# Performance work log

Measured on AMD Instinct MI355X. Metric: run time of the kernel, lower is better.

The kernel has to match this reference:

```python
import jax, jax.numpy as jnp
import numpy as np

TAU = 0.5


def _l2norm(x):
    return x / jnp.linalg.norm(x, axis=1, keepdims=True)


def _project(z, W1, b1, W2, b2):
    h = jax.nn.elu(z @ W1.T + b1)
    return h @ W2.T + b2


def _semi_loss(h1, h2):
    # cos sim via row-normalized matmul
    n1 = _l2norm(h1)
    n2 = _l2norm(h2)
    between = jnp.exp((n1 @ n2.T) / TAU)  # [N, N]
    refl = jnp.exp((n1 @ n1.T) / TAU)     # [N, N]
    pos = jnp.diagonal(between)
    denom = refl.sum(axis=1) + between.sum(axis=1) + pos \
        - jnp.diagonal(refl) - jnp.diagonal(between)
    return -jnp.log(pos / denom)


def setup_inputs() -> dict:
    key = jax.random.key(0)
    k1, k2, k3, k4 = jax.random.split(key, 4)
    N, D, P = 12288, 256, 256
    z1 = jax.random.normal(k1, (N, D), dtype=jnp.float32)
    z2 = jax.random.normal(k2, (N, D), dtype=jnp.float32)
    W1 = jax.random.normal(k3, (P, D), dtype=jnp.float32) * (1.0 / np.sqrt(D))
    b1 = jnp.zeros((P,), dtype=jnp.float32)
    W2 = jax.random.normal(k4, (D, P), dtype=jnp.float32) * (1.0 / np.sqrt(P))
    b2 = jnp.zeros((D,), dtype=jnp.float32)
    return {"z1": z1, "z2": z2, "W1": W1, "b1": b1, "W2": W2, "b2": b2}


def reference(z1, z2, W1, b1, W2, b2):
    h1 = _project(z1, W1, b1, W2, b2)
    h2 = _project(z2, W1, b1, W2, b2)
    l1 = _semi_loss(h1, h2)
    l2 = _semi_loss(h2, h1)
    return ((l1 + l2) * 0.5).mean()
```

## Files before the change

kernel.cpp:

```cpp
#include <hip/hip_runtime.h>
#include <hip/hip_bf16.h>
#include <hip/hip_fp8.h>


#define NROWS 12288
#define TWO_N 24576
#define KDIM 256
#define BM 128
#define BK 32
#define NTILE 192
#define PAIRS 96
#define SLOTS 16
#define FB 48
#define LOG2E 1.4426950408889634f
#define SIMSCALE 1.6986436f
#define LN2F 0.6931471805599453f

#if __has_builtin(__builtin_amdgcn_exp2f)
#define EXP2F(x) __builtin_amdgcn_exp2f(x)
#else
#define EXP2F(x) exp2f(x)
#endif

typedef __bf16 bf16x8 __attribute__((ext_vector_type(8)));
typedef __bf16 bf16x4v __attribute__((ext_vector_type(4)));
typedef float f32x4 __attribute__((ext_vector_type(4)));
typedef int i32x4 __attribute__((ext_vector_type(4)));
typedef int i32x8 __attribute__((ext_vector_type(8)));
typedef unsigned char uchar;

typedef const __attribute__((address_space(1))) void* gptr_t;
typedef __attribute__((address_space(3))) void* lptr_t;

__device__ __forceinline__ bf16x8 read_frag(const __bf16* lds, int rowbase,
                                            int tile, int l) {
  int r = rowbase + tile * 16 + (l & 15);
  int q = l >> 4;
  int blk = q ^ (r & 3);
  return *(const bf16x8*)(lds + r * 32 + blk * 8);
}

__global__ void cast_w_kernel(const float* __restrict__ W1,
                              const float* __restrict__ W2,
                              __bf16* __restrict__ W1b,
                              __bf16* __restrict__ W2b) {
  const int n4w = KDIM * KDIM / 4;
  int i = blockIdx.x * blockDim.x + threadIdx.x;
  const float* src;
  __bf16* dst;
  int j;
  if (i < n4w) {
    src = W1; dst = W1b; j = i;
  } else if (i < 2 * n4w) {
    src = W2; dst = W2b; j = i - n4w;
  } else {
    return;
  }
  float4 v = *(const float4*)(src + (size_t)j * 4);
  bf16x4v o;
  o[0] = (__bf16)v.x; o[1] = (__bf16)v.y; o[2] = (__bf16)v.z; o[3] = (__bf16)v.w;
  *(bf16x4v*)(dst + (size_t)j * 4) = o;
}

__device__ __forceinline__ uchar fp8_byte(float x) {
#if __has_builtin(__builtin_amdgcn_cvt_pk_fp8_f32)
  int v = __builtin_amdgcn_cvt_pk_fp8_f32(x, 0.f, 0, false);
  return (uchar)(v & 0xFF);
#else
  __hip_fp8_e4m3 qv(x);
  return qv.__x;
#endif
}

__global__ __launch_bounds__(256, 2) void mlp_kernel(
    const float* __restrict__ z1, const float* __restrict__ z2,
    const __bf16* __restrict__ W1b, const __bf16* __restrict__ W2b,
    const float* __restrict__ b1, const float* __restrict__ b2,
    uchar* __restrict__ Nq) {
  __shared__ __align__(16) __bf16 Zs[64 * BK];
  __shared__ __align__(16) __bf16 Ws[KDIM * BK];
  __shared__ __align__(16) __bf16 Ts[8 * 64 * 32];
  __shared__ float ssred[4][64];
  __shared__ float invred[64];
  uchar* qbuf = (uchar*)Ts;
  int tid = threadIdx.x;
  int w = tid >> 6, l = tid & 63;
  int q = l >> 4, rx = l & 15;
  int i0 = blockIdx.x * 64;
  int wbcol = w * 64;
  const float* zrow = (i0 < NROWS) ? (z1 + (size_t)i0 * KDIM)
                                   : (z2 + (size_t)(i0 - NROWS) * KDIM);

  auto stageW = [&](const __bf16* Wb, int ks) {
#pragma unroll
    for (int t = 0; t < 4; ++t) {
      int c = w * 4 + t;
      int rr = l >> 2, c2 = l & 3;
      int r = c * 16 + rr;
      int src = c2 ^ (r & 3);
      const __bf16* ga = Wb + (size_t)r * KDIM + ks * BK + src * 8;
      __builtin_amdgcn_global_load_lds((gptr_t)ga, (lptr_t)(Ws + c * 512),
                                       16, 0, 0);
    }
  };
  const int zr = tid >> 2, zblk = tid & 3;
  const int zsrc = zblk ^ (zr & 3);
  auto loadZ = [&](int ks, float4& v0, float4& v1) {
    const float* zp = zrow + (size_t)zr * KDIM + ks * BK + zsrc * 8;
    v0 = *(const float4*)zp;
    v1 = *(const float4*)(zp + 4);
  };

  f32x4 acc[4][4] = {};
  float4 zv0, zv1;
  loadZ(0, zv0, zv1);
  for (int ks = 0; ks < 8; ++ks) {
    __syncthreads();
    bf16x8 zo;
    zo[0] = (__bf16)zv0.x; zo[1] = (__bf16)zv0.y;
    zo[2] = (__bf16)zv0.z; zo[3] = (__bf16)zv0.w;
    zo[4] = (__bf16)zv1.x; zo[5] = (__bf16)zv1.y;
    zo[6] = (__bf16)zv1.z; zo[7] = (__bf16)zv1.w;
    *(bf16x8*)(Zs + zr * 32 + zblk * 8) = zo;
    stageW(W1b, ks);
    if (ks + 1 < 8) loadZ(ks + 1, zv0, zv1);
    __syncthreads();
    bf16x8 aF[4], bF[4];
#pragma unroll
    for (int mi = 0; mi < 4; ++mi) aF[mi] = read_frag(Zs, 0, mi, l);
#pragma unroll
    for (int ni = 0; ni < 4; ++ni) bF[ni] = read_frag(Ws, wbcol, ni, l);
#pragma unroll
    for (int mi = 0; mi < 4; ++mi)
#pragma unroll
      for (int ni = 0; ni < 4; ++ni)
        acc[mi][ni] = __builtin_amdgcn_mfma_f32_16x16x32_bf16(
            aF[mi], bF[ni], acc[mi][ni], 0, 0, 0);
  }

  float bias1[4];
#pragma unroll
  for (int ni = 0; ni < 4; ++ni) bias1[ni] = b1[wbcol + ni * 16 + rx];
#pragma unroll
  for (int mi = 0; mi < 4; ++mi)
#pragma unroll
    for (int ni = 0; ni < 4; ++ni)
#pragma unroll
      for (int v = 0; v < 4; ++v) {
        int row = mi * 16 + q * 4 + v;
        int col = wbcol + ni * 16 + rx;
        float x = acc[mi][ni][v] + bias1[ni];
        x = x > 0.f ? x : (EXP2F(x * LOG2E) - 1.f);
        int ks2 = col >> 5, c32 = col & 31;
        Ts[ks2 * 2048 + row * 32 + (((c32 >> 3) ^ (row & 3)) << 3) +
           (col & 7)] = (__bf16)x;
      }

#pragma unroll
  for (int mi = 0; mi < 4; ++mi)
#pragma unroll
    for (int ni = 0; ni < 4; ++ni) acc[mi][ni] = (f32x4){0.f, 0.f, 0.f, 0.f};
  for (int ks = 0; ks < 8; ++ks) {
    __syncthreads();
    stageW(W2b, ks);
    __syncthreads();
    bf16x8 aF[4], bF[4];
#pragma unroll
    for (int mi = 0; mi < 4; ++mi)
      aF[mi] = read_frag(Ts + ks * 2048, 0, mi, l);
#pragma unroll
    for (int ni = 0; ni < 4; ++ni) bF[ni] = read_frag(Ws, wbcol, ni, l);
#pragma unroll
    for (int mi = 0; mi < 4; ++mi)
#pragma unroll
      for (int ni = 0; ni < 4; ++ni)
        acc[mi][ni] = __builtin_amdgcn_mfma_f32_16x16x32_bf16(
            aF[mi], bF[ni], acc[mi][ni], 0, 0, 0);
  }

  float bias2[4];
#pragma unroll
  for (int ni = 0; ni < 4; ++ni) bias2[ni] = b2[wbcol + ni * 16 + rx];
  float ss[4][4] = {};
#pragma unroll
  for (int mi = 0; mi < 4; ++mi)
#pragma unroll
    for (int ni = 0; ni < 4; ++ni)
#pragma unroll
      for (int v = 0; v < 4; ++v) {
        float x = acc[mi][ni][v] + bias2[ni];
        acc[mi][ni][v] = x;
        ss[mi][v] += x * x;
      }
#pragma unroll
  for (int mi = 0; mi < 4; ++mi)
#pragma unroll
    for (int v = 0; v < 4; ++v) {
      float x = ss[mi][v];
      x += __shfl_xor(x, 1, 64);
      x += __shfl_xor(x, 2, 64);
      x += __shfl_xor(x, 4, 64);
      x += __shfl_xor(x, 8, 64);
      if (rx == 0) ssred[w][mi * 16 + q * 4 + v] = x;
    }
  __syncthreads();
  if (tid < 64)
    invred[tid] = rsqrtf(ssred[0][tid] + ssred[1][tid] + ssred[2][tid] +
                         ssred[3][tid]) * SIMSCALE;
  __syncthreads();

#pragma unroll
  for (int mi = 0; mi < 4; ++mi)
#pragma unroll
    for (int v = 0; v < 4; ++v) {
      int row = mi * 16 + q * 4 + v;
      float iv = invred[row];
#pragma unroll
      for (int ni = 0; ni < 4; ++ni)
        qbuf[row * KDIM + wbcol + ni * 16 + rx] =
            fp8_byte(acc[mi][ni][v] * iv);
    }
  __syncthreads();
  size_t base = (size_t)i0 * KDIM;
#pragma unroll
  for (int it = 0; it < 8; ++it) {
    int idx = it * 2048 + tid * 8;
    *(uint2*)(Nq + base + idx) = *(const uint2*)(qbuf + idx);
  }
}

__global__ __launch_bounds__(256, 2) void sim_kernel(
    const uchar* __restrict__ Nq, float* __restrict__ Rlow,
    float* __restrict__ Rhigh, float* __restrict__ Dsame,
    float* __restrict__ Dcross) {
  __shared__ __align__(16) uchar Bs[2][BM * KDIM];
  int tid = threadIdx.x;
  int w = tid >> 6, l = tid & 63;
  int q = l >> 4;
  int rx = l & 15;
  int b = blockIdx.x;
  int p = b >> 4;
  int s = b & 15;
  const int I1 = p, I2 = NTILE - 1 - p;
  const int L1 = NTILE - I1;
  int fstart = (s == 0) ? 0 : 13 + (s - 1) * 12;
  int fend = fstart + ((s == 0) ? 13 : 12);
  int warow = (w >> 1) * 64;
  int wbcol = (w & 1) * 64;

  unsigned off0[8];
#pragma unroll
  for (int t = 0; t < 8; ++t) {
    int ch = w * 8 + t;
    int r = ch * 4 + (l >> 4);
    int c = l & 15;
    int src = c ^ (r & 15);
    off0[t] = (unsigned)(r * KDIM + src * 16);
  }
  auto jtile_of = [&](int F) { return (F < L1) ? (I1 + F) : (F - 1); };
  auto atile_of = [&](int F) { return (F < L1) ? I1 : I2; };

  auto stage = [&](int F, int bi) {
    unsigned jo = (unsigned)(jtile_of(F) * (BM * KDIM));
#pragma unroll
    for (int t = 0; t < 8; ++t) {
      const uchar* ga = Nq + (size_t)(jo + off0[t]);
      uchar* la = Bs[bi] + (w * 8 + t) * 1024;
      __builtin_amdgcn_global_load_lds((gptr_t)ga, (lptr_t)la, 16, 0, 0);
    }
  };

  i32x8 aF[4][2];
  auto load_aF = [&](int Atile) {
#pragma unroll
    for (int mi = 0; mi < 4; ++mi) {
      const uchar* ap = Nq +
          (size_t)(Atile * BM + warow + mi * 16 + rx) * KDIM + q * 32;
#pragma unroll
      for (int hf = 0; hf < 2; ++hf)
        aF[mi][hf] = *(const i32x8*)(ap + hf * 128);
    }
  };

  int rdo[2][2];
#pragma unroll
  for (int hf = 0; hf < 2; ++hf) {
    int kb = hf * 8 + 2 * q;
    rdo[hf][0] = (kb ^ rx) << 4;
    rdo[hf][1] = ((kb + 1) ^ rx) << 4;
  }

  f32x4 rs4[4] = {};
  f32x4 cs4[4];
  int pend = 0;
  float* pendR = nullptr;
  int pendBase = 0;

  auto flushrs = [&](int Atile, int h) {
    float* R = h ? Rhigh : Rlow;
#pragma unroll
    for (int mi = 0; mi < 4; ++mi)
#pragma unroll
      for (int v = 0; v < 4; ++v) {
        float x = rs4[mi][v];
        x += __shfl_xor(x, 1, 64);
        x += __shfl_xor(x, 2, 64);
        x += __shfl_xor(x, 4, 64);
        x += __shfl_xor(x, 8, 64);
        if (rx == 0)
          atomicAdd(&R[Atile * BM + warow + mi * 16 + q * 4 + v], x);
        rs4[mi][v] = 0.f;
      }
  };
  auto flushcs = [&]() {
#pragma unroll
    for (int nj = 0; nj < 4; ++nj) {
      float c = (cs4[nj][0] + cs4[nj][1]) + (cs4[nj][2] + cs4[nj][3]);
      c += __shfl_xor(c, 16, 64);
      c += __shfl_xor(c, 32, 64);
      if (q == 0)
        atomicAdd(&pendR[pendBase + wbcol + nj * 16 + rx], c);
    }
    pend = 0;
  };

  const f32x4 Z4 = {0.f, 0.f, 0.f, 0.f};

  int Aprev = atile_of(fstart);
  int hprev = (jtile_of(fstart) >= NTILE / 2) ? 1 : 0;
  load_aF(Aprev);
  stage(fstart, 0);

  for (int f = fstart; f < fend; ++f) {
    int bi = (f - fstart) & 1;
    __syncthreads();
    if (f + 1 < fend) stage(f + 1, bi ^ 1);
    if (pend) flushcs();

    int Atile = atile_of(f);
    int Jt = jtile_of(f);
    int h = (Jt >= NTILE / 2) ? 1 : 0;
    if (Atile != Aprev) {
      flushrs(Aprev, hprev);
      load_aF(Atile);
      Aprev = Atile;
      hprev = h;
    } else if (h != hprev) {
      flushrs(Aprev, hprev);
      hprev = h;
    }

    bool dsame = (Jt == Atile);
    bool dcross = (Jt == Atile + NTILE / 2);
    float* Rcol = (Atile >= NTILE / 2) ? Rhigh : Rlow;

    const uchar* bL = Bs[bi] + (size_t)(wbcol + rx) * KDIM;
    const uchar* p00 = bL + rdo[0][0];
    const uchar* p01 = bL + rdo[0][1];
    const uchar* p10 = bL + rdo[1][0];
    const uchar* p11 = bL + rdo[1][1];

#pragma unroll
    for (int nj = 0; nj < 4; ++nj) {
      const int no = nj * 4096;
      i32x8 bF0 = __builtin_shufflevector(*(const i32x4*)(p00 + no),
                                          *(const i32x4*)(p01 + no),
                                          0, 1, 2, 3, 4, 5, 6, 7);
      i32x8 bF1 = __builtin_shufflevector(*(const i32x4*)(p10 + no),
                                          *(const i32x4*)(p11 + no),
                                          0, 1, 2, 3, 4, 5, 6, 7);
      f32x4 acc[4];
#pragma unroll
      for (int mi = 0; mi < 4; ++mi)
        acc[mi] = __builtin_amdgcn_mfma_scale_f32_16x16x128_f8f6f4(
            aF[mi][0], bF0, Z4, 0, 0, 0, 0x7F7F7F7F, 0, 0x7F7F7F7F);
#pragma unroll
      for (int mi = 0; mi < 4; ++mi)
        acc[mi] = __builtin_amdgcn_mfma_scale_f32_16x16x128_f8f6f4(
            aF[mi][1], bF1, acc[mi], 0, 0, 0, 0x7F7F7F7F, 0, 0x7F7F7F7F);
#pragma unroll
      for (int mi = 0; mi < 4; ++mi) {
        f32x4 e4;
        e4[0] = EXP2F(acc[mi][0]);
        e4[1] = EXP2F(acc[mi][1]);
        e4[2] = EXP2F(acc[mi][2]);
        e4[3] = EXP2F(acc[mi][3]);
        rs4[mi] += e4;
        cs4[nj] = (mi == 0) ? e4 : (cs4[nj] + e4);
      }

      if (dsame | dcross) {
        float* D = dsame ? Dsame : Dcross;
#pragma unroll
        for (int mi = 0; mi < 4; ++mi)
#pragma unroll
          for (int v = 0; v < 4; ++v) {
            int li = warow + mi * 16 + q * 4 + v;
            int lj = wbcol + nj * 16 + rx;
            if (li == lj) D[Atile * BM + li] = acc[mi][v];
          }
      }
    }

    if (!dsame) {
      pend = 1;
      pendR = Rcol;
      pendBase = Jt * BM;
    }
  }

  if (pend) flushcs();
  flushrs(Aprev, hprev);
}

__global__ void finalize1_kernel(const float* __restrict__ Rlow,
                                 const float* __restrict__ Rhigh,
                                 const float* __restrict__ Dsame,
                                 const float* __restrict__ Dcross,
                                 float* __restrict__ partial) {
  __shared__ float red[256];
  int k = blockIdx.x * 256 + threadIdx.x;
  float d1 = Rlow[k] + Rhigh[k] - EXP2F(Dsame[k]);
  float d2 = Rhigh[NROWS + k] + Rlow[NROWS + k] - EXP2F(Dsame[NROWS + k]);
  float acc = 0.5f * (logf(d1) + logf(d2)) - LN2F * Dcross[k];
  red[threadIdx.x] = acc;
  __syncthreads();
  for (int s = 128; s > 0; s >>= 1) {
    if (threadIdx.x < s) red[threadIdx.x] += red[threadIdx.x + s];
    __syncthreads();
  }
  if (threadIdx.x == 0) partial[blockIdx.x] = red[0];
}

__global__ void finalize2_kernel(const float* __restrict__ partial,
                                 float* __restrict__ out) {
  float x = (threadIdx.x < FB) ? partial[threadIdx.x] : 0.f;
#pragma unroll
  for (int s = 32; s > 0; s >>= 1) x += __shfl_down(x, s, 64);
  if (threadIdx.x == 0) out[0] = x / (float)NROWS;
}

extern "C" void kernel_launch(void* const* d_in, const int* in_sizes, int n_in,
                              void* d_out, int out_size, void* d_ws,
                              size_t ws_size, hipStream_t stream) {
  const float* z1 = (const float*)d_in[0];
  const float* z2 = (const float*)d_in[1];
  const float* W1 = (const float*)d_in[2];
  const float* b1 = (const float*)d_in[3];
  const float* W2 = (const float*)d_in[4];
  const float* b2 = (const float*)d_in[5];
  float* out = (float*)d_out;

  char* ws = (char*)d_ws;
  size_t off = 0;
  auto alloc = [&](size_t bytes) -> void* {
    void* p = ws + off;
    off += (bytes + 255) & ~(size_t)255;
    return p;
  };
  __bf16* W1b  = (__bf16*)alloc((size_t)KDIM * KDIM * 2);
  __bf16* W2b  = (__bf16*)alloc((size_t)KDIM * KDIM * 2);
  uchar*  Nq   = (uchar*)alloc((size_t)TWO_N * KDIM);
  float*  Rlow = (float*)alloc((size_t)TWO_N * 4);
  float*  Rhigh= (float*)alloc((size_t)TWO_N * 4);
  float*  Dsame= (float*)alloc((size_t)TWO_N * 4);
  float*  Dcross=(float*)alloc((size_t)NROWS * 4);
  float*  partial=(float*)alloc((size_t)FB * 4);

  hipMemsetAsync(Rlow, 0, (size_t)2 * TWO_N * 4, stream);

  int n4w = KDIM * KDIM / 4;
  cast_w_kernel<<<(2 * n4w + 255) / 256, 256, 0, stream>>>(W1, W2, W1b, W2b);

  mlp_kernel<<<TWO_N / 64, 256, 0, stream>>>(z1, z2, W1b, W2b, b1, b2, Nq);

  sim_kernel<<<PAIRS * SLOTS, 256, 0, stream>>>(Nq, Rlow, Rhigh, Dsame,
                                                Dcross);
  finalize1_kernel<<<FB, 256, 0, stream>>>(Rlow, Rhigh, Dsame, Dcross, partial);
  finalize2_kernel<<<1, 64, 0, stream>>>(partial, out);
}
```

Measured before the change: 210.2 us.

## Split sim kernel into MFMA producer and exp/reduce consumer warps

Result: slower. 279.3 us (+32.9%).

```diff
diff --git a/kernel.cpp b/kernel.cpp
--- a/kernel.cpp
+++ b/kernel.cpp
@@ -10,7 +10,6 @@
 #define BK 32
 #define NTILE 192
 #define PAIRS 96
-#define SLOTS 16
 #define FB 48
 #define LOG2E 1.4426950408889634f
 #define SIMSCALE 1.6986436f
@@ -229,43 +228,46 @@
   }
 }
 
-__global__ __launch_bounds__(256, 2) void sim_kernel(
+__global__ __launch_bounds__(512, 2) void sim_kernel(
     const uchar* __restrict__ Nq, float* __restrict__ Rlow,
     float* __restrict__ Rhigh, float* __restrict__ Dsame,
     float* __restrict__ Dcross) {
   __shared__ __align__(16) uchar Bs[2][BM * KDIM];
+  __shared__ __align__(16) float4 Ab[2][4][512];
   int tid = threadIdx.x;
   int w = tid >> 6, l = tid & 63;
+  bool prod = (w < 4);
+  int wq = w & 3;
   int q = l >> 4;
   int rx = l & 15;
   int b = blockIdx.x;
-  int p = b >> 4;
-  int s = b & 15;
+  int p = b >> 3;
+  int s = b & 7;
   const int I1 = p, I2 = NTILE - 1 - p;
   const int L1 = NTILE - I1;
-  int fstart = (s == 0) ? 0 : 13 + (s - 1) * 12;
-  int fend = fstart + ((s == 0) ? 13 : 12);
-  int warow = (w >> 1) * 64;
-  int wbcol = (w & 1) * 64;
-
-  unsigned off0[8];
-#pragma unroll
-  for (int t = 0; t < 8; ++t) {
-    int ch = w * 8 + t;
-    int r = ch * 4 + (l >> 4);
-    int c = l & 15;
-    int src = c ^ (r & 15);
-    off0[t] = (unsigned)(r * KDIM + src * 16);
-  }
+  int fstart = (s == 0) ? 0 : 25 + (s - 1) * 24;
+  int fend = fstart + ((s == 0) ? 25 : 24);
+  const int T = fend - fstart;
+  int warow = (wq >> 1) * 64;
+  int wbcol = (wq & 1) * 64;
+
   auto jtile_of = [&](int F) { return (F < L1) ? (I1 + F) : (F - 1); };
   auto atile_of = [&](int F) { return (F < L1) ? I1 : I2; };
 
+  unsigned off0[8];
+#pragma unroll
+  for (int t = 0; t < 8; ++t) {
+    int ch = wq * 8 + t;
+    int r = ch * 4 + q;
+    int src = rx ^ (r & 15);
+    off0[t] = (unsigned)(r * KDIM + src * 16);
+  }
   auto stage = [&](int F, int bi) {
     unsigned jo = (unsigned)(jtile_of(F) * (BM * KDIM));
 #pragma unroll
     for (int t = 0; t < 8; ++t) {
       const uchar* ga = Nq + (size_t)(jo + off0[t]);
-      uchar* la = Bs[bi] + (w * 8 + t) * 1024;
+      uchar* la = Bs[bi] + (wq * 8 + t) * 1024;
       __builtin_amdgcn_global_load_lds((gptr_t)ga, (lptr_t)la, 16, 0, 0);
     }
   };
@@ -281,7 +283,6 @@
         aF[mi][hf] = *(const i32x8*)(ap + hf * 128);
     }
   };
-
   int rdo[2][2];
 #pragma unroll
   for (int hf = 0; hf < 2; ++hf) {
@@ -289,12 +290,44 @@
     rdo[hf][0] = (kb ^ rx) << 4;
     rdo[hf][1] = ((kb + 1) ^ rx) << 4;
   }
+  const f32x4 Z4 = {0.f, 0.f, 0.f, 0.f};
+
+  auto produce = [&](int ht) {
+    int fl = ht >> 1;
+    int njbase = (ht & 1) * 2;
+    const uchar* bL = Bs[fl & 1] + (size_t)(wbcol + rx) * KDIM;
+#pragma unroll
+    for (int njh = 0; njh < 2; ++njh) {
+      const int no = (njbase + njh) * 4096;
+      i32x8 bF0 = __builtin_shufflevector(
+          *(const i32x4*)(bL + no + rdo[0][0]),
+          *(const i32x4*)(bL + no + rdo[0][1]), 0, 1, 2, 3, 4, 5, 6, 7);
+      i32x8 bF1 = __builtin_shufflevector(
+          *(const i32x4*)(bL + no + rdo[1][0]),
+          *(const i32x4*)(bL + no + rdo[1][1]), 0, 1, 2, 3, 4, 5, 6, 7);
+      f32x4 acc[4];
+#pragma unroll
+      for (int mi = 0; mi < 4; ++mi)
+        acc[mi] = __builtin_amdgcn_mfma_scale_f32_16x16x128_f8f6f4(
+            aF[mi][0], bF0, Z4, 0, 0, 0, 0x7F7F7F7F, 0, 0x7F7F7F7F);
+#pragma unroll
+      for (int mi = 0; mi < 4; ++mi)
+        acc[mi] = __builtin_amdgcn_mfma_scale_f32_16x16x128_f8f6f4(
+            aF[mi][1], bF1, acc[mi], 0, 0, 0, 0x7F7F7F7F, 0, 0x7F7F7F7F);
+#pragma unroll
+      for (int mi = 0; mi < 4; ++mi)
+        Ab[ht & 1][wq][(njh * 4 + mi) * 64 + l] =
+            (float4){acc[mi][0], acc[mi][1], acc[mi][2], acc[mi][3]};
+    }
+  };
 
   f32x4 rs4[4] = {};
   f32x4 cs4[4];
   int pend = 0;
   float* pendR = nullptr;
   int pendBase = 0;
+  int Aprev = atile_of(fstart);
+  int hprev = (jtile_of(fstart) >= NTILE / 2) ? 1 : 0;
 
   auto flushrs = [&](int Atile, int h) {
     float* R = h ? Rhigh : Rlow;
@@ -324,93 +357,92 @@
     pend = 0;
   };
 
-  const f32x4 Z4 = {0.f, 0.f, 0.f, 0.f};
-
-  int Aprev = atile_of(fstart);
-  int hprev = (jtile_of(fstart) >= NTILE / 2) ? 1 : 0;
-  load_aF(Aprev);
-  stage(fstart, 0);
-
-  for (int f = fstart; f < fend; ++f) {
-    int bi = (f - fstart) & 1;
-    __syncthreads();
-    if (f + 1 < fend) stage(f + 1, bi ^ 1);
-    if (pend) flushcs();
-
+  auto consume = [&](int g) {
+    int fl = g >> 1;
+    int f = fstart + fl;
+    int half = g & 1;
     int Atile = atile_of(f);
     int Jt = jtile_of(f);
-    int h = (Jt >= NTILE / 2) ? 1 : 0;
-    if (Atile != Aprev) {
-      flushrs(Aprev, hprev);
-      load_aF(Atile);
-      Aprev = Atile;
-      hprev = h;
-    } else if (h != hprev) {
-      flushrs(Aprev, hprev);
-      hprev = h;
-    }
-
     bool dsame = (Jt == Atile);
     bool dcross = (Jt == Atile + NTILE / 2);
-    float* Rcol = (Atile >= NTILE / 2) ? Rhigh : Rlow;
-
-    const uchar* bL = Bs[bi] + (size_t)(wbcol + rx) * KDIM;
-    const uchar* p00 = bL + rdo[0][0];
-    const uchar* p01 = bL + rdo[0][1];
-    const uchar* p10 = bL + rdo[1][0];
-    const uchar* p11 = bL + rdo[1][1];
-
-#pragma unroll
-    for (int nj = 0; nj < 4; ++nj) {
-      const int no = nj * 4096;
-      i32x8 bF0 = __builtin_shufflevector(*(const i32x4*)(p00 + no),
-                                          *(const i32x4*)(p01 + no),
-                                          0, 1, 2, 3, 4, 5, 6, 7);
-      i32x8 bF1 = __builtin_shufflevector(*(const i32x4*)(p10 + no),
-                                          *(const i32x4*)(p11 + no),
-                                          0, 1, 2, 3, 4, 5, 6, 7);
-      f32x4 acc[4];
-#pragma unroll
-      for (int mi = 0; mi < 4; ++mi)
-        acc[mi] = __builtin_amdgcn_mfma_scale_f32_16x16x128_f8f6f4(
-            aF[mi][0], bF0, Z4, 0, 0, 0, 0x7F7F7F7F, 0, 0x7F7F7F7F);
-#pragma unroll
-      for (int mi = 0; mi < 4; ++mi)
-        acc[mi] = __builtin_amdgcn_mfma_scale_f32_16x16x128_f8f6f4(
-            aF[mi][1], bF1, acc[mi], 0, 0, 0, 0x7F7F7F7F, 0, 0x7F7F7F7F);
+    if (half == 0) {
+      int h = (Jt >= NTILE / 2) ? 1 : 0;
+      if (pend) flushcs();
+      if (Atile != Aprev) {
+        flushrs(Aprev, hprev);
+        Aprev = Atile;
+        hprev = h;
+      } else if (h != hprev) {
+        flushrs(Aprev, hprev);
+        hprev = h;
+      }
+    }
+#pragma unroll
+    for (int njh = 0; njh < 2; ++njh) {
+      int nj = half * 2 + njh;
+      f32x4 e4sum = {0.f, 0.f, 0.f, 0.f};
 #pragma unroll
       for (int mi = 0; mi < 4; ++mi) {
-        f32x4 e4;
-        e4[0] = EXP2F(acc[mi][0]);
-        e4[1] = EXP2F(acc[mi][1]);
-        e4[2] = EXP2F(acc[mi][2]);
-        e4[3] = EXP2F(acc[mi][3]);
-        rs4[mi] += e4;
-        cs4[nj] = (mi == 0) ? e4 : (cs4[nj] + e4);
-      }
-
-      if (dsame | dcross) {
-        float* D = dsame ? Dsame : Dcross;
-#pragma unroll
-        for (int mi = 0; mi < 4; ++mi)
+        float4 a = Ab[g & 1][wq][(njh * 4 + mi) * 64 + l];
+        if (dsame | dcross) {
+          float* D = dsame ? Dsame : Dcross;
 #pragma unroll
           for (int v = 0; v < 4; ++v) {
             int li = warow + mi * 16 + q * 4 + v;
             int lj = wbcol + nj * 16 + rx;
-            if (li == lj) D[Atile * BM + li] = acc[mi][v];
+            float av = (v == 0) ? a.x : (v == 1) ? a.y : (v == 2) ? a.z : a.w;
+            if (li == lj) D[Atile * BM + li] = av;
           }
+        }
+        f32x4 e4;
+        e4[0] = EXP2F(a.x);
+        e4[1] = EXP2F(a.y);
+        e4[2] = EXP2F(a.z);
+        e4[3] = EXP2F(a.w);
+        rs4[mi] += e4;
+        e4sum += e4;
       }
-    }
-
-    if (!dsame) {
+      cs4[nj] = (half == 0 && njh == 0 && false) ? e4sum : e4sum;
+      cs4[nj] = e4sum;
+    }
+    if (half == 1 && !dsame) {
       pend = 1;
-      pendR = Rcol;
+      pendR = (Atile >= NTILE / 2) ? Rhigh : Rlow;
       pendBase = Jt * BM;
     }
-  }
-
-  if (pend) flushcs();
-  flushrs(Aprev, hprev);
+  };
+
+  if (prod) stage(fstart, 0);
+  __syncthreads();
+  if (prod) {
+    load_aF(atile_of(fstart));
+    produce(0);
+    if (T > 1) stage(fstart + 1, 1);
+  }
+
+  for (int g = 0; g < 2 * T; ++g) {
+    __syncthreads();
+    int ht = g + 1;
+    if (prod) {
+      if (ht < 2 * T) {
+        int fl = ht >> 1;
+        if ((ht & 1) == 0) {
+          int At = atile_of(fstart + fl);
+          int Ap = atile_of(fstart + fl - 1);
+          if (At != Ap) load_aF(At);
+          if (fl + 1 < T) stage(fstart + fl + 1, (fl + 1) & 1);
+        }
+        produce(ht);
+      }
+    } else {
+      consume(g);
+    }
+  }
+
+  if (!prod) {
+    if (pend) flushcs();
+    flushrs(Aprev, hprev);
+  }
 }
 
 __global__ void finalize1_kernel(const float* __restrict__ Rlow,
@@ -474,8 +506,7 @@
 
   mlp_kernel<<<TWO_N / 64, 256, 0, stream>>>(z1, z2, W1b, W2b, b1, b2, Nq);
 
-  sim_kernel<<<PAIRS * SLOTS, 256, 0, stream>>>(Nq, Rlow, Rhigh, Dsame,
-                                                Dcross);
+  sim_kernel<<<PAIRS * 8, 512, 0, stream>>>(Nq, Rlow, Rhigh, Dsame, Dcross);
   finalize1_kernel<<<FB, 256, 0, stream>>>(Rlow, Rhigh, Dsame, Dcross, partial);
   finalize2_kernel<<<1, 64, 0, stream>>>(partial, out);
 }
```

## Split sim tiles into 128x64 half-tiles with each wave owning 32 rows

Applied to the files above, without the earlier changes.

Measured after the change: 202.0 us. -3.9%, faster.

```diff
diff --git a/kernel.cpp b/kernel.cpp
--- a/kernel.cpp
+++ b/kernel.cpp
@@ -233,7 +233,7 @@
     const uchar* __restrict__ Nq, float* __restrict__ Rlow,
     float* __restrict__ Rhigh, float* __restrict__ Dsame,
     float* __restrict__ Dcross) {
-  __shared__ __align__(16) uchar Bs[2][BM * KDIM];
+  __shared__ __align__(16) uchar Bs[2][64 * KDIM];
   int tid = threadIdx.x;
   int w = tid >> 6, l = tid & 63;
   int q = l >> 4;
@@ -243,37 +243,36 @@
   int s = b & 15;
   const int I1 = p, I2 = NTILE - 1 - p;
   const int L1 = NTILE - I1;
-  int fstart = (s == 0) ? 0 : 13 + (s - 1) * 12;
-  int fend = fstart + ((s == 0) ? 13 : 12);
-  int warow = (w >> 1) * 64;
-  int wbcol = (w & 1) * 64;
-
-  unsigned off0[8];
-#pragma unroll
-  for (int t = 0; t < 8; ++t) {
-    int ch = w * 8 + t;
-    int r = ch * 4 + (l >> 4);
-    int c = l & 15;
-    int src = c ^ (r & 15);
+  int gstart = (s == 0) ? 0 : 26 + (s - 1) * 24;
+  int gend = gstart + ((s == 0) ? 26 : 24);
+  int warow = w * 32;
+
+  unsigned off0[4];
+#pragma unroll
+  for (int t = 0; t < 4; ++t) {
+    int ch = w * 4 + t;
+    int r = ch * 4 + q;
+    int src = rx ^ (r & 15);
     off0[t] = (unsigned)(r * KDIM + src * 16);
   }
   auto jtile_of = [&](int F) { return (F < L1) ? (I1 + F) : (F - 1); };
   auto atile_of = [&](int F) { return (F < L1) ? I1 : I2; };
-
-  auto stage = [&](int F, int bi) {
-    unsigned jo = (unsigned)(jtile_of(F) * (BM * KDIM));
-#pragma unroll
-    for (int t = 0; t < 8; ++t) {
+  auto j64_of = [&](int G) { return jtile_of(G >> 1) * 2 + (G & 1); };
+
+  auto stage = [&](int G, int bi) {
+    unsigned jo = (unsigned)(j64_of(G) * (64 * KDIM));
+#pragma unroll
+    for (int t = 0; t < 4; ++t) {
       const uchar* ga = Nq + (size_t)(jo + off0[t]);
-      uchar* la = Bs[bi] + (w * 8 + t) * 1024;
+      uchar* la = Bs[bi] + (w * 4 + t) * 1024;
       __builtin_amdgcn_global_load_lds((gptr_t)ga, (lptr_t)la, 16, 0, 0);
     }
   };
 
-  i32x8 aF[4][2];
+  i32x8 aF[2][2];
   auto load_aF = [&](int Atile) {
 #pragma unroll
-    for (int mi = 0; mi < 4; ++mi) {
+    for (int mi = 0; mi < 2; ++mi) {
       const uchar* ap = Nq +
           (size_t)(Atile * BM + warow + mi * 16 + rx) * KDIM + q * 32;
 #pragma unroll
@@ -290,7 +289,7 @@
     rdo[hf][1] = ((kb + 1) ^ rx) << 4;
   }
 
-  f32x4 rs4[4] = {};
+  f32x4 rs4[2] = {};
   f32x4 cs4[4];
   int pend = 0;
   float* pendR = nullptr;
@@ -299,7 +298,7 @@
   auto flushrs = [&](int Atile, int h) {
     float* R = h ? Rhigh : Rlow;
 #pragma unroll
-    for (int mi = 0; mi < 4; ++mi)
+    for (int mi = 0; mi < 2; ++mi)
 #pragma unroll
       for (int v = 0; v < 4; ++v) {
         float x = rs4[mi][v];
@@ -319,27 +318,29 @@
       c += __shfl_xor(c, 16, 64);
       c += __shfl_xor(c, 32, 64);
       if (q == 0)
-        atomicAdd(&pendR[pendBase + wbcol + nj * 16 + rx], c);
+        atomicAdd(&pendR[pendBase + nj * 16 + rx], c);
     }
     pend = 0;
   };
 
   const f32x4 Z4 = {0.f, 0.f, 0.f, 0.f};
 
-  int Aprev = atile_of(fstart);
-  int hprev = (jtile_of(fstart) >= NTILE / 2) ? 1 : 0;
+  int Aprev = atile_of(gstart >> 1);
+  int hprev = (j64_of(gstart) >= NTILE) ? 1 : 0;
   load_aF(Aprev);
-  stage(fstart, 0);
-
-  for (int f = fstart; f < fend; ++f) {
-    int bi = (f - fstart) & 1;
-    __syncthreads();
-    if (f + 1 < fend) stage(f + 1, bi ^ 1);
+  stage(gstart, 0);
+
+  for (int g = gstart; g < gend; ++g) {
+    int bi = (g - gstart) & 1;
+    __syncthreads();
+    if (g + 1 < gend) stage(g + 1, bi ^ 1);
     if (pend) flushcs();
 
-    int Atile = atile_of(f);
-    int Jt = jtile_of(f);
-    int h = (Jt >= NTILE / 2) ? 1 : 0;
+    int F = g >> 1, half = g & 1;
+    int Atile = atile_of(F);
+    int Jt = jtile_of(F);
+    int j64 = Jt * 2 + half;
+    int h = (j64 >= NTILE) ? 1 : 0;
     if (Atile != Aprev) {
       flushrs(Aprev, hprev);
       load_aF(Atile);
@@ -354,7 +355,7 @@
     bool dcross = (Jt == Atile + NTILE / 2);
     float* Rcol = (Atile >= NTILE / 2) ? Rhigh : Rlow;
 
-    const uchar* bL = Bs[bi] + (size_t)(wbcol + rx) * KDIM;
+    const uchar* bL = Bs[bi] + (size_t)rx * KDIM;
     const uchar* p00 = bL + rdo[0][0];
     const uchar* p01 = bL + rdo[0][1];
     const uchar* p10 = bL + rdo[1][0];
@@ -369,17 +370,17 @@
       i32x8 bF1 = __builtin_shufflevector(*(const i32x4*)(p10 + no),
                                           *(const i32x4*)(p11 + no),
                                           0, 1, 2, 3, 4, 5, 6, 7);
-      f32x4 acc[4];
-#pragma unroll
-      for (int mi = 0; mi < 4; ++mi)
+      f32x4 acc[2];
+#pragma unroll
+      for (int mi = 0; mi < 2; ++mi)
         acc[mi] = __builtin_amdgcn_mfma_scale_f32_16x16x128_f8f6f4(
             aF[mi][0], bF0, Z4, 0, 0, 0, 0x7F7F7F7F, 0, 0x7F7F7F7F);
 #pragma unroll
-      for (int mi = 0; mi < 4; ++mi)
+      for (int mi = 0; mi < 2; ++mi)
         acc[mi] = __builtin_amdgcn_mfma_scale_f32_16x16x128_f8f6f4(
             aF[mi][1], bF1, acc[mi], 0, 0, 0, 0x7F7F7F7F, 0, 0x7F7F7F7F);
 #pragma unroll
-      for (int mi = 0; mi < 4; ++mi) {
+      for (int mi = 0; mi < 2; ++mi) {
         f32x4 e4;
         e4[0] = EXP2F(acc[mi][0]);
         e4[1] = EXP2F(acc[mi][1]);
@@ -392,11 +393,11 @@
       if (dsame | dcross) {
         float* D = dsame ? Dsame : Dcross;
 #pragma unroll
-        for (int mi = 0; mi < 4; ++mi)
+        for (int mi = 0; mi < 2; ++mi)
 #pragma unroll
           for (int v = 0; v < 4; ++v) {
             int li = warow + mi * 16 + q * 4 + v;
-            int lj = wbcol + nj * 16 + rx;
+            int lj = half * 64 + nj * 16 + rx;
             if (li == lj) D[Atile * BM + li] = acc[mi][v];
           }
       }
@@ -405,7 +406,7 @@
     if (!dsame) {
       pend = 1;
       pendR = Rcol;
-      pendBase = Jt * BM;
+      pendBase = j64 * 64;
     }
   }
 
```
